# Kernel optimization log

Measured on AMD Instinct MI355X. Metric: run time of the kernel, lower is better.

Reference implementation:

```python
import jax, jax.numpy as jnp
import numpy as np

B, S, H = 4, 2048, 1024
NH, HD = 8, 128  # num_heads, head_dim

def setup_inputs() -> dict:
    key = jax.random.key(0)
    ks = jax.random.split(key, 5)
    scale = 1.0 / np.sqrt(H)
    return {
        "hidden_states": jax.random.normal(ks[0], (B, S, H), dtype=jnp.float32),
        "Wq": jax.random.normal(ks[1], (H, H), dtype=jnp.float32) * scale,
        "Wk": jax.random.normal(ks[2], (H, H), dtype=jnp.float32) * scale,
        "Wv": jax.random.normal(ks[3], (H, H), dtype=jnp.float32) * scale,
        "Wo": jax.random.normal(ks[4], (H, H), dtype=jnp.float32) * scale,
    }

def reference(hidden_states, Wq, Wk, Wv, Wo):
    # projections (torch Linear: x @ W.T), weights stored [out, in]
    q = hidden_states @ Wq.T
    k = hidden_states @ Wk.T
    v = hidden_states @ Wv.T
    # [B, NH, S, HD]
    q = q.reshape(B, S, NH, HD).transpose(0, 2, 1, 3)
    k = k.reshape(B, S, NH, HD).transpose(0, 2, 1, 3)
    v = v.reshape(B, S, NH, HD).transpose(0, 2, 1, 3)
    scale = 1.0 / jnp.sqrt(jnp.asarray(HD, dtype=q.dtype))
    scores = jnp.einsum("bhqd,bhkd->bhqk", q, k) * scale
    # softmax in fp32, cast back to input dtype (matches torch F.softmax dtype=float32)
    attn = jax.nn.softmax(scores.astype(jnp.float32), axis=-1).astype(q.dtype)
    out = jnp.einsum("bhqk,bhkd->bhqd", attn, v)
    out = out.transpose(0, 2, 1, 3).reshape(B, S, H)
    return out @ Wo.T
```

## Files before the change

kernel.cpp:

```cpp
#include <hip/hip_runtime.h>
#include <stdint.h>

#define Bz  4
#define Sz  2048
#define Hz  1024
#define NHz 8
#define HDz 128
#define Mz  (Bz*Sz)

typedef __attribute__((ext_vector_type(8))) short bf16x8;
typedef __attribute__((ext_vector_type(4))) float f32x4;

__device__ __forceinline__ unsigned short f2bf(float x) {
  union { float f; unsigned int u; } c; c.f = x;
  unsigned int u = c.u;
  return (unsigned short)((u + 0x7FFFu + ((u >> 16) & 1u)) >> 16);
}

__device__ __forceinline__ void gl2lds16(const unsigned short* g, unsigned short* l) {
  __builtin_amdgcn_global_load_lds(
      (const __attribute__((address_space(1))) unsigned int*)g,
      (__attribute__((address_space(3))) unsigned int*)l, 16, 0, 0);
}

__global__ __launch_bounds__(256)
void cvt_kernel(const float* __restrict__ in, unsigned short* __restrict__ out, int n) {
  const int n4 = n >> 2;
  for (int i = blockIdx.x * blockDim.x + threadIdx.x; i < n4; i += gridDim.x * blockDim.x) {
    float4 v = ((const float4*)in)[i];
    ushort4 o;
    o.x = f2bf(v.x); o.y = f2bf(v.y); o.z = f2bf(v.z); o.w = f2bf(v.w);
    ((ushort4*)out)[i] = o;
  }
}

__global__ __launch_bounds__(256)
void cvt4_kernel(const float* __restrict__ w0, const float* __restrict__ w1,
                 const float* __restrict__ w2, const float* __restrict__ w3,
                 unsigned short* __restrict__ o0, unsigned short* __restrict__ o1,
                 unsigned short* __restrict__ o2, unsigned short* __restrict__ o3) {
  const int which = blockIdx.y;
  const float* in = (which == 0) ? w0 : (which == 1) ? w1 : (which == 2) ? w2 : w3;
  unsigned short* out = (which == 0) ? o0 : (which == 1) ? o1 : (which == 2) ? o2 : o3;
  const int n4 = (Hz * Hz) >> 2;
  for (int i = blockIdx.x * blockDim.x + threadIdx.x; i < n4; i += gridDim.x * blockDim.x) {
    float4 v = ((const float4*)in)[i];
    ushort4 o;
    o.x = f2bf(v.x); o.y = f2bf(v.y); o.z = f2bf(v.z); o.w = f2bf(v.w);
    ((ushort4*)out)[i] = o;
  }
}

template<bool BF16_OUT, bool VT_OUT>
__global__ __launch_bounds__(256)
void gemm_bt_k(const unsigned short* __restrict__ A,
               const unsigned short* __restrict__ Bw,
               void* __restrict__ Cv, float alpha)
{
  __shared__ __align__(16) unsigned short Asm[128 * 64];
  __shared__ __align__(16) unsigned short Bsm[128 * 64];
  const int tid = threadIdx.x;
  const int w  = tid >> 6, l = tid & 63;
  const int lc = l & 15,  lg = l >> 4;
  const int wr = w >> 1,  wc = w & 1;
  const int bm = blockIdx.x * 128;
  const int bn = blockIdx.y * 128;

  f32x4 acc[4][4];
#pragma unroll
  for (int i = 0; i < 4; i++)
#pragma unroll
    for (int j = 0; j < 4; j++) acc[i][j] = (f32x4){0.f, 0.f, 0.f, 0.f};

  const int srow = w * 32 + (l >> 3);
  const int scol = (l & 7) * 8;

  for (int kt = 0; kt < 16; kt++) {
    const int k0 = kt * 64;
    __syncthreads();
#pragma unroll
    for (int i = 0; i < 4; i++) {
      gl2lds16(A  + (size_t)(bm + srow + i * 8) * Hz + k0 + scol, &Asm[(w * 32 + i * 8) * 64]);
      gl2lds16(Bw + (size_t)(bn + srow + i * 8) * Hz + k0 + scol, &Bsm[(w * 32 + i * 8) * 64]);
    }
    __syncthreads();

#pragma unroll
    for (int kk = 0; kk < 2; kk++) {
      bf16x8 af[4], bf[4];
#pragma unroll
      for (int t = 0; t < 4; t++) {
        af[t] = *(const bf16x8*)&Asm[(wr * 64 + t * 16 + lc) * 64 + kk * 32 + lg * 8];
        bf[t] = *(const bf16x8*)&Bsm[(wc * 64 + t * 16 + lc) * 64 + kk * 32 + lg * 8];
      }
#pragma unroll
      for (int mt = 0; mt < 4; mt++)
#pragma unroll
        for (int nt = 0; nt < 4; nt++)
          acc[mt][nt] = __builtin_amdgcn_mfma_f32_16x16x32_bf16(af[mt], bf[nt], acc[mt][nt], 0, 0, 0);
    }
  }

#pragma unroll
  for (int mt = 0; mt < 4; mt++) {
#pragma unroll
    for (int nt = 0; nt < 4; nt++) {
      const int row0 = bm + wr * 64 + mt * 16 + lg * 4;
      const int col  = bn + wc * 64 + nt * 16 + lc;
      if (VT_OUT) {
        unsigned short* Vt = (unsigned short*)Cv;
        ushort4 pk;
        pk.x = f2bf(acc[mt][nt][0] * alpha);
        pk.y = f2bf(acc[mt][nt][1] * alpha);
        pk.z = f2bf(acc[mt][nt][2] * alpha);
        pk.w = f2bf(acc[mt][nt][3] * alpha);
        const size_t idx = ((size_t)((row0 >> 11) << 10) + col) * Sz + (row0 & 2047);
        *(ushort4*)&Vt[idx] = pk;
      } else if (BF16_OUT) {
        unsigned short* C = (unsigned short*)Cv;
#pragma unroll
        for (int r = 0; r < 4; r++)
          C[(size_t)(row0 + r) * Hz + col] = f2bf(acc[mt][nt][r] * alpha);
      } else {
        float* C = (float*)Cv;
#pragma unroll
        for (int r = 0; r < 4; r++)
          C[(size_t)(row0 + r) * Hz + col] = acc[mt][nt][r] * alpha;
      }
    }
  }
}

__global__ __launch_bounds__(256, 2)
void attn_fwd(const unsigned short* __restrict__ Q,
              const unsigned short* __restrict__ K,
              const unsigned short* __restrict__ Vt,
              unsigned short* __restrict__ O)
{
  const int bid = blockIdx.x;
  const int wg  = (bid & 7) * 64 + (bid >> 3);
  const int qb  = wg & 15;
  const int bh  = wg >> 4;
  const int b = bh >> 3, nh = bh & 7;
  const int w = threadIdx.x >> 6, l = threadIdx.x & 63;
  const int lc = l & 15, lg = l >> 4;

  __shared__ __align__(16) unsigned short Ksm[2][64 * 128];
  __shared__ __align__(16) unsigned short Vsm[128 * 64];
  __shared__ __align__(16) unsigned short Psm[4][16 * 64];

  bf16x8 qf[2][4];
#pragma unroll
  for (int mt = 0; mt < 2; mt++)
#pragma unroll
    for (int ks = 0; ks < 4; ks++)
      qf[mt][ks] = *(const bf16x8*)(Q + ((size_t)b * Sz + qb * 128 + w * 32 + mt * 16 + lc) * Hz
                                      + nh * HDz + ks * 32 + lg * 8);

  const unsigned short* Kbase = K  + (size_t)b * Sz * Hz + nh * HDz;
  const unsigned short* Vbase = Vt + (size_t)bh * HDz * Sz;

  f32x4 acc[2][8];
#pragma unroll
  for (int mt = 0; mt < 2; mt++)
#pragma unroll
    for (int i = 0; i < 8; i++) acc[mt][i] = (f32x4){0.f, 0.f, 0.f, 0.f};
  float mrow[2][4], lrow[2][4];
#pragma unroll
  for (int mt = 0; mt < 2; mt++)
#pragma unroll
    for (int r = 0; r < 4; r++) { mrow[mt][r] = -1e30f; lrow[mt][r] = 0.f; }

  #define STAGE_K(BUF, KT) {                                                          \
    _Pragma("unroll")                                                                 \
    for (int i = 0; i < 4; i++) {                                                     \
      const int r = w * 16 + i * 4 + (l >> 4);                                        \
      gl2lds16(Kbase + (size_t)((KT) * 64 + r) * Hz + (((l & 15) ^ (r & 7)) * 8),     \
               &Ksm[BUF][(w * 16 + i * 4) * 128]);                                    \
    } }
  #define STAGE_V(KT) {                                                               \
    _Pragma("unroll")                                                                 \
    for (int i = 0; i < 4; i++) {                                                     \
      const int r = w * 32 + i * 8 + (l >> 3);                                        \
      gl2lds16(Vbase + (size_t)r * Sz + (KT) * 64 + (((l & 7) ^ (r & 7)) * 8),        \
               &Vsm[(w * 32 + i * 8) * 64]);                                          \
    } }

  int cur = 0;
  STAGE_K(0, 0);
  __syncthreads();

  for (int kt = 0; kt < Sz / 64; kt++) {
    STAGE_V(kt);
    if (kt < Sz / 64 - 1) STAGE_K(cur ^ 1, kt + 1);

    f32x4 s[2][4];
#pragma unroll
    for (int mt = 0; mt < 2; mt++)
#pragma unroll
      for (int nt = 0; nt < 4; nt++) s[mt][nt] = (f32x4){0.f, 0.f, 0.f, 0.f};
#pragma unroll
    for (int ks = 0; ks < 4; ks++) {
#pragma unroll
      for (int nt = 0; nt < 4; nt++) {
        bf16x8 kf = *(const bf16x8*)&Ksm[cur][(nt * 16 + lc) * 128 + (((ks * 4 + lg) ^ (lc & 7)) * 8)];
#pragma unroll
        for (int mt = 0; mt < 2; mt++)
          s[mt][nt] = __builtin_amdgcn_mfma_f32_16x16x32_bf16(qf[mt][ks], kf, s[mt][nt], 0, 0, 0);
      }
    }

#pragma unroll
    for (int mt = 0; mt < 2; mt++) {
#pragma unroll
      for (int r = 0; r < 4; r++) {
        float tm = fmaxf(fmaxf(s[mt][0][r], s[mt][1][r]), fmaxf(s[mt][2][r], s[mt][3][r]));
        tm = fmaxf(tm, __shfl_xor(tm, 1));
        tm = fmaxf(tm, __shfl_xor(tm, 2));
        tm = fmaxf(tm, __shfl_xor(tm, 4));
        tm = fmaxf(tm, __shfl_xor(tm, 8));
        if (tm > mrow[mt][r] + 8.0f) {
          const float sc = exp2f(mrow[mt][r] - tm);
          mrow[mt][r] = tm;
          lrow[mt][r] *= sc;
#pragma unroll
          for (int nt = 0; nt < 8; nt++) acc[mt][nt][r] *= sc;
        }
        float rs = 0.f;
#pragma unroll
        for (int nt = 0; nt < 4; nt++) {
          float p = exp2f(s[mt][nt][r] - mrow[mt][r]);
          s[mt][nt][r] = p;
          rs += p;
        }
        rs += __shfl_xor(rs, 1);
        rs += __shfl_xor(rs, 2);
        rs += __shfl_xor(rs, 4);
        rs += __shfl_xor(rs, 8);
        lrow[mt][r] += rs;
      }
    }

    bf16x8 pf[2][2];
#pragma unroll
    for (int mt = 0; mt < 2; mt++) {
#pragma unroll
      for (int nt = 0; nt < 4; nt++)
#pragma unroll
        for (int r = 0; r < 4; r++) {
          const int row = lg * 4 + r;
          const int ch  = (nt * 2 + (lc >> 3)) ^ (row & 7);
          Psm[w][row * 64 + ch * 8 + (lc & 7)] = f2bf(s[mt][nt][r]);
        }
#pragma unroll
      for (int kk = 0; kk < 2; kk++)
        pf[mt][kk] = *(const bf16x8*)&Psm[w][lc * 64 + (((kk * 4 + lg) ^ (lc & 7)) * 8)];
    }

    __syncthreads();

#pragma unroll
    for (int kk = 0; kk < 2; kk++) {
#pragma unroll
      for (int nt = 0; nt < 8; nt++) {
        bf16x8 vf = *(const bf16x8*)&Vsm[(nt * 16 + lc) * 64 + (((kk * 4 + lg) ^ (lc & 7)) * 8)];
        acc[0][nt] = __builtin_amdgcn_mfma_f32_16x16x32_bf16(pf[0][kk], vf, acc[0][nt], 0, 0, 0);
        acc[1][nt] = __builtin_amdgcn_mfma_f32_16x16x32_bf16(pf[1][kk], vf, acc[1][nt], 0, 0, 0);
      }
    }

    __syncthreads();
    cur ^= 1;
  }

#pragma unroll
  for (int mt = 0; mt < 2; mt++)
#pragma unroll
    for (int nt = 0; nt < 8; nt++)
#pragma unroll
      for (int r = 0; r < 4; r++) {
        const size_t row = (size_t)b * Sz + qb * 128 + w * 32 + mt * 16 + lg * 4 + r;
        O[row * Hz + nh * HDz + nt * 16 + lc] = f2bf(acc[mt][nt][r] / lrow[mt][r]);
      }
}

extern "C" void kernel_launch(void* const* d_in, const int* in_sizes, int n_in,
                              void* d_out, int out_size, void* d_ws, size_t ws_size,
                              hipStream_t stream) {
  const float* hs = (const float*)d_in[0];
  const float* Wq = (const float*)d_in[1];
  const float* Wk = (const float*)d_in[2];
  const float* Wv = (const float*)d_in[3];
  const float* Wo = (const float*)d_in[4];

  const size_t NEL = (size_t)Mz * Hz;
  const size_t WEL = (size_t)Hz * Hz;

  unsigned short* p = (unsigned short*)d_ws;
  unsigned short* hs_bf = p; p += NEL;
  unsigned short* Wq_bf = p; p += WEL;
  unsigned short* Wk_bf = p; p += WEL;
  unsigned short* Wv_bf = p; p += WEL;
  unsigned short* Wo_bf = p; p += WEL;
  unsigned short* Qb    = p; p += NEL;
  unsigned short* Kb    = p; p += NEL;
  unsigned short* Vtb   = p; p += NEL;
  unsigned short* Ob    = hs_bf;

  cvt_kernel<<<2048, 256, 0, stream>>>(hs, hs_bf, (int)NEL);
  cvt4_kernel<<<dim3(512, 4), 256, 0, stream>>>(Wq, Wk, Wv, Wo,
                                                Wq_bf, Wk_bf, Wv_bf, Wo_bf);

  dim3 gg(Mz / 128, Hz / 128);
  const float qscale = 0.08838834764831845f * 1.44269504088896340736f;
  gemm_bt_k<true,  false><<<gg, 256, 0, stream>>>(hs_bf, Wq_bf, Qb,  qscale);
  gemm_bt_k<true,  false><<<gg, 256, 0, stream>>>(hs_bf, Wk_bf, Kb,  1.0f);
  gemm_bt_k<true,  true ><<<gg, 256, 0, stream>>>(hs_bf, Wv_bf, Vtb, 1.0f);

  attn_fwd<<<512, 256, 0, stream>>>(Qb, Kb, Vtb, Ob);

  gemm_bt_k<false, false><<<gg, 256, 0, stream>>>(Ob, Wo_bf, (float*)d_out, 1.0f);
}
```

Baseline: 350.3 us.

## Merge QKV GEMMs, load V directly from global, raise attention occupancy

The three projection GEMMs become one launch using blockIdx.z to pick the weight, which cuts launch overhead and improves tail fill. In attention, V is no longer staged through LDS; each wave reads V fragments straight from global memory. That frees LDS and removes a barrier, so launch bounds rise to 4 blocks per CU. It also adds s_setprio around the MFMA sections and uses a reciprocal in the epilogue, at the risk of uncoalesced, latency-exposed global V reads inside the inner loop.

```diff
diff --git a/kernel.cpp b/kernel.cpp
--- a/kernel.cpp
+++ b/kernel.cpp
@@ -51,55 +51,63 @@
   }
 }
 
-template<bool BF16_OUT, bool VT_OUT>
+#define GEMM_PROLOG()                                                           \
+  __shared__ __align__(16) unsigned short Asm[128 * 64];                        \
+  __shared__ __align__(16) unsigned short Bsm[128 * 64];                        \
+  const int tid = threadIdx.x;                                                  \
+  const int w  = tid >> 6, l = tid & 63;                                        \
+  const int lc = l & 15,  lg = l >> 4;                                          \
+  const int wr = w >> 1,  wc = w & 1;                                           \
+  const int bm = blockIdx.x * 128;                                              \
+  const int bn = blockIdx.y * 128;                                              \
+  f32x4 acc[4][4];                                                              \
+  _Pragma("unroll")                                                             \
+  for (int i = 0; i < 4; i++)                                                   \
+    _Pragma("unroll")                                                           \
+    for (int j = 0; j < 4; j++) acc[i][j] = (f32x4){0.f, 0.f, 0.f, 0.f};        \
+  const int srow = w * 32 + (l >> 3);                                           \
+  const int scol = (l & 7) * 8;                                                 \
+  for (int kt = 0; kt < 16; kt++) {                                             \
+    const int k0 = kt * 64;                                                     \
+    __syncthreads();                                                            \
+    _Pragma("unroll")                                                           \
+    for (int i = 0; i < 4; i++) {                                               \
+      gl2lds16(A  + (size_t)(bm + srow + i * 8) * Hz + k0 + scol,               \
+               &Asm[(w * 32 + i * 8) * 64]);                                    \
+      gl2lds16(Bw + (size_t)(bn + srow + i * 8) * Hz + k0 + scol,               \
+               &Bsm[(w * 32 + i * 8) * 64]);                                    \
+    }                                                                           \
+    __syncthreads();                                                            \
+    _Pragma("unroll")                                                           \
+    for (int kk = 0; kk < 2; kk++) {                                            \
+      bf16x8 af[4], bf[4];                                                      \
+      _Pragma("unroll")                                                         \
+      for (int t = 0; t < 4; t++) {                                             \
+        af[t] = *(const bf16x8*)&Asm[(wr*64 + t*16 + lc)*64 + kk*32 + lg*8];    \
+        bf[t] = *(const bf16x8*)&Bsm[(wc*64 + t*16 + lc)*64 + kk*32 + lg*8];    \
+      }                                                                         \
+      _Pragma("unroll")                                                         \
+      for (int mt = 0; mt < 4; mt++)                                            \
+        _Pragma("unroll")                                                       \
+        for (int nt = 0; nt < 4; nt++)                                          \
+          acc[mt][nt] = __builtin_amdgcn_mfma_f32_16x16x32_bf16(                \
+              af[mt], bf[nt], acc[mt][nt], 0, 0, 0);                            \
+    }                                                                           \
+  }
+
 __global__ __launch_bounds__(256)
-void gemm_bt_k(const unsigned short* __restrict__ A,
-               const unsigned short* __restrict__ Bw,
-               void* __restrict__ Cv, float alpha)
+void gemm_qkv(const unsigned short* __restrict__ A,
+              const unsigned short* __restrict__ W0,
+              const unsigned short* __restrict__ W1,
+              const unsigned short* __restrict__ W2,
+              unsigned short* __restrict__ Qo,
+              unsigned short* __restrict__ Ko,
+              unsigned short* __restrict__ Vto, float qscale)
 {
-  __shared__ __align__(16) unsigned short Asm[128 * 64];
-  __shared__ __align__(16) unsigned short Bsm[128 * 64];
-  const int tid = threadIdx.x;
-  const int w  = tid >> 6, l = tid & 63;
-  const int lc = l & 15,  lg = l >> 4;
-  const int wr = w >> 1,  wc = w & 1;
-  const int bm = blockIdx.x * 128;
-  const int bn = blockIdx.y * 128;
-
-  f32x4 acc[4][4];
-#pragma unroll
-  for (int i = 0; i < 4; i++)
-#pragma unroll
-    for (int j = 0; j < 4; j++) acc[i][j] = (f32x4){0.f, 0.f, 0.f, 0.f};
-
-  const int srow = w * 32 + (l >> 3);
-  const int scol = (l & 7) * 8;
-
-  for (int kt = 0; kt < 16; kt++) {
-    const int k0 = kt * 64;
-    __syncthreads();
-#pragma unroll
-    for (int i = 0; i < 4; i++) {
-      gl2lds16(A  + (size_t)(bm + srow + i * 8) * Hz + k0 + scol, &Asm[(w * 32 + i * 8) * 64]);
-      gl2lds16(Bw + (size_t)(bn + srow + i * 8) * Hz + k0 + scol, &Bsm[(w * 32 + i * 8) * 64]);
-    }
-    __syncthreads();
-
-#pragma unroll
-    for (int kk = 0; kk < 2; kk++) {
-      bf16x8 af[4], bf[4];
-#pragma unroll
-      for (int t = 0; t < 4; t++) {
-        af[t] = *(const bf16x8*)&Asm[(wr * 64 + t * 16 + lc) * 64 + kk * 32 + lg * 8];
-        bf[t] = *(const bf16x8*)&Bsm[(wc * 64 + t * 16 + lc) * 64 + kk * 32 + lg * 8];
-      }
-#pragma unroll
-      for (int mt = 0; mt < 4; mt++)
-#pragma unroll
-        for (int nt = 0; nt < 4; nt++)
-          acc[mt][nt] = __builtin_amdgcn_mfma_f32_16x16x32_bf16(af[mt], bf[nt], acc[mt][nt], 0, 0, 0);
-    }
-  }
+  const int z = blockIdx.z;
+  const unsigned short* Bw = (z == 0) ? W0 : (z == 1) ? W1 : W2;
+  const float alpha = (z == 0) ? qscale : 1.0f;
+  GEMM_PROLOG()
 
 #pragma unroll
   for (int mt = 0; mt < 4; mt++) {
@@ -107,31 +115,43 @@
     for (int nt = 0; nt < 4; nt++) {
       const int row0 = bm + wr * 64 + mt * 16 + lg * 4;
       const int col  = bn + wc * 64 + nt * 16 + lc;
-      if (VT_OUT) {
-        unsigned short* Vt = (unsigned short*)Cv;
+      if (z == 2) {
         ushort4 pk;
-        pk.x = f2bf(acc[mt][nt][0] * alpha);
-        pk.y = f2bf(acc[mt][nt][1] * alpha);
-        pk.z = f2bf(acc[mt][nt][2] * alpha);
-        pk.w = f2bf(acc[mt][nt][3] * alpha);
+        pk.x = f2bf(acc[mt][nt][0]);
+        pk.y = f2bf(acc[mt][nt][1]);
+        pk.z = f2bf(acc[mt][nt][2]);
+        pk.w = f2bf(acc[mt][nt][3]);
         const size_t idx = ((size_t)((row0 >> 11) << 10) + col) * Sz + (row0 & 2047);
-        *(ushort4*)&Vt[idx] = pk;
-      } else if (BF16_OUT) {
-        unsigned short* C = (unsigned short*)Cv;
+        *(ushort4*)&Vto[idx] = pk;
+      } else {
+        unsigned short* C = (z == 0) ? Qo : Ko;
 #pragma unroll
         for (int r = 0; r < 4; r++)
           C[(size_t)(row0 + r) * Hz + col] = f2bf(acc[mt][nt][r] * alpha);
-      } else {
-        float* C = (float*)Cv;
-#pragma unroll
-        for (int r = 0; r < 4; r++)
-          C[(size_t)(row0 + r) * Hz + col] = acc[mt][nt][r] * alpha;
-      }
-    }
-  }
-}
-
-__global__ __launch_bounds__(256, 2)
+      }
+    }
+  }
+}
+
+__global__ __launch_bounds__(256)
+void gemm_out(const unsigned short* __restrict__ A,
+              const unsigned short* __restrict__ Bw,
+              float* __restrict__ C)
+{
+  GEMM_PROLOG()
+#pragma unroll
+  for (int mt = 0; mt < 4; mt++)
+#pragma unroll
+    for (int nt = 0; nt < 4; nt++) {
+      const int row0 = bm + wr * 64 + mt * 16 + lg * 4;
+      const int col  = bn + wc * 64 + nt * 16 + lc;
+#pragma unroll
+      for (int r = 0; r < 4; r++)
+        C[(size_t)(row0 + r) * Hz + col] = acc[mt][nt][r];
+    }
+}
+
+__global__ __launch_bounds__(256, 4)
 void attn_fwd(const unsigned short* __restrict__ Q,
               const unsigned short* __restrict__ K,
               const unsigned short* __restrict__ Vt,
@@ -146,7 +166,6 @@
   const int lc = l & 15, lg = l >> 4;
 
   __shared__ __align__(16) unsigned short Ksm[2][64 * 128];
-  __shared__ __align__(16) unsigned short Vsm[128 * 64];
   __shared__ __align__(16) unsigned short Psm[4][16 * 64];
 
   bf16x8 qf[2][4];
@@ -178,20 +197,12 @@
       gl2lds16(Kbase + (size_t)((KT) * 64 + r) * Hz + (((l & 15) ^ (r & 7)) * 8),     \
                &Ksm[BUF][(w * 16 + i * 4) * 128]);                                    \
     } }
-  #define STAGE_V(KT) {                                                               \
-    _Pragma("unroll")                                                                 \
-    for (int i = 0; i < 4; i++) {                                                     \
-      const int r = w * 32 + i * 8 + (l >> 3);                                        \
-      gl2lds16(Vbase + (size_t)r * Sz + (KT) * 64 + (((l & 7) ^ (r & 7)) * 8),        \
-               &Vsm[(w * 32 + i * 8) * 64]);                                          \
-    } }
 
   int cur = 0;
   STAGE_K(0, 0);
   __syncthreads();
 
   for (int kt = 0; kt < Sz / 64; kt++) {
-    STAGE_V(kt);
     if (kt < Sz / 64 - 1) STAGE_K(cur ^ 1, kt + 1);
 
     f32x4 s[2][4];
@@ -199,6 +210,7 @@
     for (int mt = 0; mt < 2; mt++)
 #pragma unroll
       for (int nt = 0; nt < 4; nt++) s[mt][nt] = (f32x4){0.f, 0.f, 0.f, 0.f};
+    __builtin_amdgcn_s_setprio(1);
 #pragma unroll
     for (int ks = 0; ks < 4; ks++) {
 #pragma unroll
@@ -209,6 +221,7 @@
           s[mt][nt] = __builtin_amdgcn_mfma_f32_16x16x32_bf16(qf[mt][ks], kf, s[mt][nt], 0, 0, 0);
       }
     }
+    __builtin_amdgcn_s_setprio(0);
 
 #pragma unroll
     for (int mt = 0; mt < 2; mt++) {
@@ -257,31 +270,35 @@
         pf[mt][kk] = *(const bf16x8*)&Psm[w][lc * 64 + (((kk * 4 + lg) ^ (lc & 7)) * 8)];
     }
 
-    __syncthreads();
-
+    __builtin_amdgcn_s_setprio(1);
 #pragma unroll
     for (int kk = 0; kk < 2; kk++) {
 #pragma unroll
       for (int nt = 0; nt < 8; nt++) {
-        bf16x8 vf = *(const bf16x8*)&Vsm[(nt * 16 + lc) * 64 + (((kk * 4 + lg) ^ (lc & 7)) * 8)];
+        bf16x8 vf = *(const bf16x8*)(Vbase + (size_t)(nt * 16 + lc) * Sz + kt * 64 + kk * 32 + lg * 8);
         acc[0][nt] = __builtin_amdgcn_mfma_f32_16x16x32_bf16(pf[0][kk], vf, acc[0][nt], 0, 0, 0);
         acc[1][nt] = __builtin_amdgcn_mfma_f32_16x16x32_bf16(pf[1][kk], vf, acc[1][nt], 0, 0, 0);
       }
     }
+    __builtin_amdgcn_s_setprio(0);
 
     __syncthreads();
     cur ^= 1;
   }
 
 #pragma unroll
-  for (int mt = 0; mt < 2; mt++)
+  for (int mt = 0; mt < 2; mt++) {
+    float inv[4];
+#pragma unroll
+    for (int r = 0; r < 4; r++) inv[r] = 1.0f / lrow[mt][r];
 #pragma unroll
     for (int nt = 0; nt < 8; nt++)
 #pragma unroll
       for (int r = 0; r < 4; r++) {
         const size_t row = (size_t)b * Sz + qb * 128 + w * 32 + mt * 16 + lg * 4 + r;
-        O[row * Hz + nh * HDz + nt * 16 + lc] = f2bf(acc[mt][nt][r] / lrow[mt][r]);
-      }
+        O[row * Hz + nh * HDz + nt * 16 + lc] = f2bf(acc[mt][nt][r] * inv[r]);
+      }
+  }
 }
 
 extern "C" void kernel_launch(void* const* d_in, const int* in_sizes, int n_in,
@@ -311,13 +328,11 @@
   cvt4_kernel<<<dim3(512, 4), 256, 0, stream>>>(Wq, Wk, Wv, Wo,
                                                 Wq_bf, Wk_bf, Wv_bf, Wo_bf);
 
-  dim3 gg(Mz / 128, Hz / 128);
   const float qscale = 0.08838834764831845f * 1.44269504088896340736f;
-  gemm_bt_k<true,  false><<<gg, 256, 0, stream>>>(hs_bf, Wq_bf, Qb,  qscale);
-  gemm_bt_k<true,  false><<<gg, 256, 0, stream>>>(hs_bf, Wk_bf, Kb,  1.0f);
-  gemm_bt_k<true,  true ><<<gg, 256, 0, stream>>>(hs_bf, Wv_bf, Vtb, 1.0f);
+  gemm_qkv<<<dim3(Mz / 128, Hz / 128, 3), 256, 0, stream>>>(
+      hs_bf, Wq_bf, Wk_bf, Wv_bf, Qb, Kb, Vtb, qscale);
 
   attn_fwd<<<512, 256, 0, stream>>>(Qb, Kb, Vtb, Ob);
 
-  gemm_bt_k<false, false><<<gg, 256, 0, stream>>>(Ob, Wo_bf, (float*)d_out, 1.0f);
-}
+  gemm_out<<<dim3(Mz / 128, Hz / 128), 256, 0, stream>>>(Ob, Wo_bf, (float*)d_out);
+}
```

Measured after the change: 728.4 us. +107.9%, slower.
